# Optimization experiments

Measured on AMD Instinct MI355X. Metric: run time of the kernel, lower is better.

The kernel has to match this reference:

```python
import jax, jax.numpy as jnp
import numpy as np

KH, KW = 3, 3
K = KH * KW
PAD, STRIDE, DIL = 1, 1, 1


def _conv(x, w, b):
    y = jax.lax.conv_general_dilated(
        x, w, (STRIDE, STRIDE), ((PAD, PAD), (PAD, PAD)),
        rhs_dilation=(DIL, DIL), dimension_numbers=('NCHW', 'OIHW', 'NCHW'))
    return y + b[None, :, None, None]


def _bilinear_gather(x, py, px):
    # x: [B,C,H,W]; py, px: float sample coords [B,K,Ho,Wo]. Zero outside bounds.
    B, C, H, W = x.shape
    y0 = jnp.floor(py)
    x0 = jnp.floor(px)
    wy1 = py - y0
    wx1 = px - x0
    wy0 = 1.0 - wy1
    wx0 = 1.0 - wx1
    xf = x.reshape(B, C, H * W)

    def g(yi, xi):
        valid = (yi >= 0) & (yi < H) & (xi >= 0) & (xi < W)
        yc = jnp.clip(yi, 0, H - 1).astype(jnp.int32)
        xc = jnp.clip(xi, 0, W - 1).astype(jnp.int32)
        idx = (yc * W + xc).reshape(B, -1)                      # [B, K*Ho*Wo]
        v = jax.vmap(lambda im, ix: im[:, ix])(xf, idx)         # [B, C, K*Ho*Wo]
        v = v.reshape(B, C, *yi.shape[1:])                      # [B,C,K,Ho,Wo]
        return v * valid[:, None].astype(x.dtype)

    return ((wy0 * wx0)[:, None] * g(y0, x0)
            + (wy0 * wx1)[:, None] * g(y0, x0 + 1)
            + (wy1 * wx0)[:, None] * g(y0 + 1, x0)
            + (wy1 * wx1)[:, None] * g(y0 + 1, x0 + 1))


def setup_inputs() -> dict:
    key = jax.random.key(0)
    k1, k2, k3 = jax.random.split(key, 3)
    B, C, H, W = 8, 256, 64, 64
    x = jax.random.normal(k1, (B, C, H, W), dtype=jnp.float32)
    # small init for offset/mask conv so predicted offsets stay modest (as in DCNv2 practice)
    w_om = jax.random.normal(k2, (3 * K, C, KH, KW), dtype=jnp.float32) * 0.01
    b_om = jnp.zeros((3 * K,), dtype=jnp.float32)
    w_dc = jax.random.normal(k3, (C, C, KH, KW), dtype=jnp.float32) * (1.0 / np.sqrt(C * K))
    b_dc = jnp.zeros((C,), dtype=jnp.float32)
    return {"x": x, "w_om": w_om, "b_om": b_om, "w_dc": w_dc, "b_dc": b_dc}


def reference(x, w_om, b_om, w_dc, b_dc):
    B, C, H, W = x.shape
    om = _conv(x, w_om, b_om)                      # [B, 3K, H, W]
    offset = om[:, :2 * K].reshape(B, K, 2, H, W)  # per-tap (dy, dx)
    mask = jax.nn.sigmoid(om[:, 2 * K:])           # [B, K, H, W]
    dy, dx = offset[:, :, 0], offset[:, :, 1]
    kh = jnp.repeat(jnp.arange(KH), KW)            # [K] kernel row index
    kw = jnp.tile(jnp.arange(KW), KH)              # [K] kernel col index
    ho = jnp.arange(H)
    wo = jnp.arange(W)
    py = ho[None, None, :, None] * STRIDE - PAD + kh[None, :, None, None] * DIL + dy
    px = wo[None, None, None, :] * STRIDE - PAD + kw[None, :, None, None] * DIL + dx
    sampled = _bilinear_gather(x, py, px)          # [B,C,K,H,W]
    sampled = sampled * mask[:, None]              # modulated (DCNv2)
    w = w_dc.reshape(w_dc.shape[0], C, K)
    out = jnp.einsum('bckhw,ock->bohw', sampled, w) + b_dc[None, :, None, None]
    return out
```

## Files before the change

kernel.cpp:

```cpp
#include <hip/hip_runtime.h>
#include <hip/hip_bf16.h>
#include <hip/hip_fp16.h>
#include <math.h>

#define BB   8
#define CIN  256
#define HH   64
#define WW   64
#define OMC  27
#define HW   (HH*WW)
#define KTOT (CIN*9)
#define NPIX 32
#define SPITCH 296
#define SSZ   (NPIX*SPITCH)
#define XP1    40
#define TPW    17
#define TBUF   4096

typedef short bf16x8 __attribute__((ext_vector_type(8)));
typedef float f32x4  __attribute__((ext_vector_type(4)));

__device__ __forceinline__ unsigned short f2bf(float f) {
    union { float f; unsigned int u; } v; v.f = f;
    unsigned int r = v.u + 0x7FFFu + ((v.u >> 16) & 1u);
    return (unsigned short)(r >> 16);
}
__device__ __forceinline__ float bflo(unsigned int a) {
    union { unsigned int u; float f; } c; c.u = a << 16; return c.f;
}
__device__ __forceinline__ float bfhi(unsigned int a) {
    union { unsigned int u; float f; } c; c.u = a & 0xFFFF0000u; return c.f;
}

__global__ __launch_bounds__(256) void wprep_kernel(
    const float* __restrict__ w_dc, unsigned short* __restrict__ wA)
{
    int e = blockIdx.x * 256 + threadIdx.x;
    int o = e / KTOT;
    int k = e - o * KTOT;
    int c   = k / 9;
    int tap = k - c * 9;
    int kp  = (c >> 5) * 288 + tap * 32 + (c & 31);
    wA[((size_t)(kp >> 3) * 256 + o) * 8 + (kp & 7)] = f2bf(w_dc[e]);
}

__global__ __launch_bounds__(256) void womprep_kernel(
    const float* __restrict__ w_om, unsigned short* __restrict__ wOmA)
{
    int e = blockIdx.x * 256 + threadIdx.x;
    int j  = e & 7;
    int t1 = e >> 3;
    int o  = t1 & 31;
    int t2 = t1 >> 5;
    int cb = t2 & 3;
    int t3 = t2 >> 2;
    int cc = t3 & 7;
    int tap = t3 >> 3;
    int c = cc * 32 + cb * 8 + j;
    float v = (o < OMC) ? w_om[(size_t)o * KTOT + c * 9 + tap] : 0.f;
    wOmA[e] = f2bf(v);
}

__global__ __launch_bounds__(512, 4) void deform_mfma_kernel(
    const float* __restrict__ x, const unsigned short* __restrict__ wOmA,
    const float* __restrict__ b_om,
    const unsigned short* __restrict__ wA, const float* __restrict__ b_dc,
    float* __restrict__ out)
{
    const int rawb = blockIdx.x;
    const int obid = ((rawb & 7) << 7) | (rawb >> 3);
    const int b    = obid >> 7;
    const int h    = (obid >> 1) & 63;
    const int w0   = (obid & 1) * NPIX;
    const int t    = threadIdx.x;
    const int wv   = t >> 6;
    const int lane = t & 63;
    const int lq   = lane >> 4;
    const int lm   = lane & 15;

    __shared__ __align__(16) unsigned short sS[2 * SSZ];
    __shared__ __align__(16) unsigned short sR[2 * TBUF * 2];
    __shared__ __align__(16) int4 s_par[9 * NPIX];

    float* som  = reinterpret_cast<float*>(sS);
    unsigned short* bufA = sR;
    unsigned short* bufB = sR + 4080;

    const size_t xb_base = (size_t)b * CIN * HW;
    const float* gx_base = x + xb_base;

    int stg[7];
#pragma unroll
    for (int i = 0; i < 7; ++i) {
        int n = t + i * 512;
        if (n < 3200) {
            int slot = n / 200;
            int rc   = n - slot * 200;
            int r    = rc / 40;
            int c    = rc - r * 40;
            int gy   = min(max(h - 2 + r, 0), HH - 1);
            int gx   = min(max(w0 - 4 + c, 0), WW - 1);
            stg[i] = (rc * TPW + slot) | (slot << 12) | ((gy * WW + gx) << 16);
        } else stg[i] = -1;
    }

    {
        f32x4 accOm = (f32x4)(0.f);
        const int mfp = (wv >> 1) & 1;
        const int nfp = wv & 1;
        const int p   = nfp * 16 + lm;
        const bf16x8* wOmV = reinterpret_cast<const bf16x8*>(wOmA);

        auto stage1 = [&](int cc, unsigned short* dst) {
            const float* gch = gx_base + (size_t)cc * 32 * HW;
#pragma unroll
            for (int i = 0; i < 7; ++i) {
                int e = t + i * 512;
                if (e < 3264) {
                    int cl  = e / 102;
                    int rc  = e - cl * 102;
                    int row = rc / 34;
                    int col = rc - row * 34;
                    int gy  = h - 1 + row;
                    int gxx = w0 - 1 + col;
                    float v = 0.f;
                    if (gy >= 0 && gy < HH && (unsigned)gxx < WW)
                        v = gch[cl * HW + gy * WW + gxx];
                    dst[rc * XP1 + cl] = f2bf(v);
                }
            }
        };

        stage1(0, bufA);
        __syncthreads();
        for (int cc = 0; cc < 8; ++cc) {
            unsigned short* cur = (cc & 1) ? bufB : bufA;
            unsigned short* nxt = (cc & 1) ? bufA : bufB;
            if (cc < 7) stage1(cc + 1, nxt);
#pragma unroll
            for (int tap = 0; tap < 9; ++tap) {
                int kh = tap / 3, kw = tap % 3;
                bf16x8 bfr = *reinterpret_cast<const bf16x8*>(
                    &cur[(kh * 34 + p + kw) * XP1 + lq * 8]);
                bf16x8 af = wOmV[(((tap * 8 + cc) * 4 + lq) * 32) + mfp * 16 + lm];
                accOm = __builtin_amdgcn_mfma_f32_16x16x32_bf16(af, bfr, accOm, 0, 0, 0);
            }
            __syncthreads();
        }

        if (wv < 4) {
#pragma unroll
            for (int r = 0; r < 4; ++r) {
                int o = mfp * 16 + lq * 4 + r;
                if (o < OMC)
                    som[o * NPIX + p] = accOm[r] + b_om[o];
            }
        }
    }
    __syncthreads();

    unsigned int* tWw = reinterpret_cast<unsigned int*>(sR);
    const unsigned int* tW = tWw;

    float L0[7], L1[7];
    auto issueStage = [&](int ch) {
        const float* gch = gx_base + (size_t)ch * 32 * HW;
#pragma unroll
        for (int i = 0; i < 7; ++i)
            if (stg[i] >= 0) {
                int sl = (stg[i] >> 12) & 0xF;
                int go = (stg[i] >> 16) & 0xFFF;
                L0[i] = gch[(size_t)(2 * sl) * HW + go];
                L1[i] = gch[(size_t)(2 * sl + 1) * HW + go];
            }
    };
    auto writeTile = [&](int buf) {
        int off = buf << 12;
#pragma unroll
        for (int i = 0; i < 7; ++i)
            if (stg[i] >= 0)
                tWw[off + (stg[i] & 0xFFF)] =
                    f2bf(L0[i]) | ((unsigned int)f2bf(L1[i]) << 16);
    };

    const int pix  = t >> 4;
    const int slot = t & 15;

    auto gather = [&](int ch) {
        const int toff = (ch & 1) << 12;
        unsigned short* sSc = sS + (ch & 1) * SSZ;
#pragma unroll 3
        for (int tap = 0; tap < 9; ++tap) {
            int idx = tap * NPIX + pix;
            int4 pv = s_par[idx];
            int pk  = pv.x;
            float2 wab = __half22float2(*reinterpret_cast<__half2*>(&pv.y));
            float2 wcd = __half22float2(*reinterpret_cast<__half2*>(&pv.z));
            float v0, v1;
            if (pk >= 0) {
                int base = toff + (pk & 0xFF) * TPW + slot;
                unsigned int a00 = tW[base];
                unsigned int a01 = tW[base + TPW];
                unsigned int a10 = tW[base + 40 * TPW];
                unsigned int a11 = tW[base + 41 * TPW];
                v0 = wab.x * bflo(a00) + wab.y * bflo(a01)
                   + wcd.x * bflo(a10) + wcd.y * bflo(a11);
                v1 = wab.x * bfhi(a00) + wab.y * bfhi(a01)
                   + wcd.x * bfhi(a10) + wcd.y * bfhi(a11);
            } else {
                int off00 = (pk >> 10) & 0xFFF;
                int d01 = (pk >> 8) & 1;
                int d10 = ((pk >> 9) & 1) * WW;
                const float* xc = x + xb_base + (size_t)(ch * 32 + 2 * slot) * HW;
                v0 = wab.x * xc[off00]       + wab.y * xc[off00 + d01]
                   + wcd.x * xc[off00 + d10] + wcd.y * xc[off00 + d10 + d01];
                xc += HW;
                v1 = wab.x * xc[off00]       + wab.y * xc[off00 + d01]
                   + wcd.x * xc[off00 + d10] + wcd.y * xc[off00 + d10 + d01];
            }
            *reinterpret_cast<unsigned int*>(
                &sSc[pix * SPITCH + tap * 32 + 2 * slot]) =
                f2bf(v0) | ((unsigned int)f2bf(v1) << 16);
        }
    };

    issueStage(0);

    for (int i = t; i < 1392; i += 512) {
        int w = (i < 696) ? (3400 + i) : (4096 + 3400 + (i - 696));
        tWw[w] = 0u;
    }

    if (t < 9 * NPIX) {
        int tap = t >> 5;
        int pix2 = t & 31;
        float dy = som[(2 * tap) * NPIX + pix2];
        float dx = som[(2 * tap + 1) * NPIX + pix2];
        float mv = som[(18 + tap) * NPIX + pix2];
        float m  = 1.f / (1.f + expf(-mv));
        float py = (float)(h - 1 + tap / 3) + dy;
        float px = (float)(w0 + pix2 - 1 + tap % 3) + dx;
        float y0f = floorf(py), x0f = floorf(px);
        float wy1 = py - y0f, wx1 = px - x0f;
        float wy0 = 1.f - wy1, wx0 = 1.f - wx1;
        int y0 = (int)y0f, x0 = (int)x0f;
        int y1 = y0 + 1, x1 = x0 + 1;
        bool yv0 = (y0 >= 0) && (y0 < HH);
        bool yv1 = (y1 >= 0) && (y1 < HH);
        bool xv0 = (x0 >= 0) && (x0 < WW);
        bool xv1 = (x1 >= 0) && (x1 < WW);
        int yc0 = min(max(y0, 0), HH - 1), yc1 = min(max(y1, 0), HH - 1);
        int xc0 = min(max(x0, 0), WW - 1), xc1 = min(max(x1, 0), WW - 1);
        float wwx = (yv0 && xv0) ? wy0 * wx0 * m : 0.f;
        float wwy = (yv0 && xv1) ? wy0 * wx1 * m : 0.f;
        float wwz = (yv1 && xv0) ? wy1 * wx0 * m : 0.f;
        float www = (yv1 && xv1) ? wy1 * wx1 * m : 0.f;
        if (xc1 == xc0) { wwx += wwy; wwy = 0.f; wwz += www; www = 0.f; }
        if (yc1 == yc0) { wwx += wwz; wwz = 0.f; wwy += www; www = 0.f; }
        bool inT = (yc0 >= h - 2) && (yc1 <= h + 2) &&
                   (xc0 >= w0 - 4) && (xc1 <= w0 + 35);
        int lb = (yc0 - (h - 2)) * 40 + (xc0 - (w0 - 4));
        int pk = (lb & 0xFF) | ((xc1 - xc0) << 8) | ((yc1 - yc0) << 9)
               | ((yc0 * WW + xc0) << 10);
        if (!inT) pk |= (int)0x80000000;
        __half2 wab = __floats2half2_rn(wwx, wwy);
        __half2 wcd = __floats2half2_rn(wwz, www);
        s_par[t] = make_int4(pk,
                             *reinterpret_cast<int*>(&wab),
                             *reinterpret_cast<int*>(&wcd), 0);
    }
    writeTile(0);
    __syncthreads();

    gather(0);
    issueStage(1);
    writeTile(1);
    __syncthreads();

    f32x4 acc[2][2];
#pragma unroll
    for (int i = 0; i < 2; ++i)
#pragma unroll
        for (int j = 0; j < 2; ++j)
            acc[i][j] = (f32x4)(0.f);

    const bf16x8* wAv = reinterpret_cast<const bf16x8*>(wA);

    for (int ch = 0; ch < 8; ++ch) {
        if (ch < 6) issueStage(ch + 2);
        if (ch < 7) gather(ch + 1);

        const unsigned short* sSc = sS + (ch & 1) * SSZ;
        const int kb_base = ch * 36;
#pragma unroll 1
        for (int ks = 0; ks < 9; ++ks) {
            bf16x8 bfr[2];
#pragma unroll
            for (int nf = 0; nf < 2; ++nf)
                bfr[nf] = *reinterpret_cast<const bf16x8*>(
                    &sSc[(nf * 16 + lm) * SPITCH + ks * 32 + lq * 8]);
#pragma unroll
            for (int mf = 0; mf < 2; ++mf) {
                int o  = wv * 32 + mf * 16 + lm;
                int kb = kb_base + ks * 4 + lq;
                bf16x8 af = wAv[(size_t)kb * 256 + o];
#pragma unroll
                for (int nf = 0; nf < 2; ++nf)
                    acc[mf][nf] = __builtin_amdgcn_mfma_f32_16x16x32_bf16(
                        af, bfr[nf], acc[mf][nf], 0, 0, 0);
            }
        }

        if (ch < 6) writeTile(ch & 1);
        __syncthreads();
    }

#pragma unroll
    for (int mf = 0; mf < 2; ++mf) {
#pragma unroll
        for (int r = 0; r < 4; ++r) {
            int o = wv * 32 + mf * 16 + lq * 4 + r;
            float bo = b_dc[o];
#pragma unroll
            for (int nf = 0; nf < 2; ++nf) {
                int p = nf * 16 + lm;
                out[((size_t)(b * 256 + o)) * HW + h * WW + w0 + p] = acc[mf][nf][r] + bo;
            }
        }
    }
}

extern "C" void kernel_launch(void* const* d_in, const int* in_sizes, int n_in,
                              void* d_out, int out_size, void* d_ws, size_t ws_size,
                              hipStream_t stream) {
    const float* x    = (const float*)d_in[0];
    const float* w_om = (const float*)d_in[1];
    const float* b_om = (const float*)d_in[2];
    const float* w_dc = (const float*)d_in[3];
    const float* b_dc = (const float*)d_in[4];
    float* out = (float*)d_out;

    unsigned short* wA   = (unsigned short*)d_ws;
    unsigned short* wOmA = (unsigned short*)((char*)d_ws + 1179648);

    wprep_kernel<<<(256 * KTOT) / 256, 256, 0, stream>>>(w_dc, wA);
    womprep_kernel<<<73728 / 256, 256, 0, stream>>>(w_om, wOmA);
    deform_mfma_kernel<<<BB * HH * 2, 512, 0, stream>>>(x, wOmA, b_om, wA, b_dc, out);
}
```

Before: 156.0 us.

## Process full 64-pixel rows per block and single-buffer the sampled tile

```diff
diff --git a/kernel.cpp b/kernel.cpp
--- a/kernel.cpp
+++ b/kernel.cpp
@@ -10,12 +10,13 @@
 #define OMC  27
 #define HW   (HH*WW)
 #define KTOT (CIN*9)
-#define NPIX 32
+#define NPIX 64
 #define SPITCH 296
-#define SSZ   (NPIX*SPITCH)
 #define XP1    40
 #define TPW    17
-#define TBUF   4096
+#define TCOLS  72
+#define TRC    360
+#define TGUARD 7360
 
 typedef short bf16x8 __attribute__((ext_vector_type(8)));
 typedef float f32x4  __attribute__((ext_vector_type(4)));
@@ -68,61 +69,60 @@
     float* __restrict__ out)
 {
     const int rawb = blockIdx.x;
-    const int obid = ((rawb & 7) << 7) | (rawb >> 3);
-    const int b    = obid >> 7;
-    const int h    = (obid >> 1) & 63;
-    const int w0   = (obid & 1) * NPIX;
+    const int obid = ((rawb & 7) << 6) | (rawb >> 3);
+    const int b    = obid >> 6;
+    const int h    = obid & 63;
     const int t    = threadIdx.x;
     const int wv   = t >> 6;
     const int lane = t & 63;
     const int lq   = lane >> 4;
     const int lm   = lane & 15;
 
-    __shared__ __align__(16) unsigned short sS[2 * SSZ];
-    __shared__ __align__(16) unsigned short sR[2 * TBUF * 2];
+    __shared__ __align__(16) unsigned short sS[NPIX * SPITCH];
+    __shared__ __align__(16) unsigned short sR[15840];
     __shared__ __align__(16) int4 s_par[9 * NPIX];
 
     float* som  = reinterpret_cast<float*>(sS);
     unsigned short* bufA = sR;
-    unsigned short* bufB = sR + 4080;
+    unsigned short* bufB = sR + 7920;
 
     const size_t xb_base = (size_t)b * CIN * HW;
     const float* gx_base = x + xb_base;
 
-    int stg[7];
-#pragma unroll
-    for (int i = 0; i < 7; ++i) {
+    int stg[12];
+#pragma unroll
+    for (int i = 0; i < 12; ++i) {
         int n = t + i * 512;
-        if (n < 3200) {
-            int slot = n / 200;
-            int rc   = n - slot * 200;
-            int r    = rc / 40;
-            int c    = rc - r * 40;
+        if (n < TRC * 16) {
+            int slot = n & 15;
+            int rc   = n >> 4;
+            int r    = rc / TCOLS;
+            int c    = rc - r * TCOLS;
             int gy   = min(max(h - 2 + r, 0), HH - 1);
-            int gx   = min(max(w0 - 4 + c, 0), WW - 1);
-            stg[i] = (rc * TPW + slot) | (slot << 12) | ((gy * WW + gx) << 16);
+            int gx   = min(max(c - 4, 0), WW - 1);
+            stg[i] = (rc * TPW + slot) | (slot << 13) | ((gy * WW + gx) << 17);
         } else stg[i] = -1;
     }
 
     {
         f32x4 accOm = (f32x4)(0.f);
-        const int mfp = (wv >> 1) & 1;
-        const int nfp = wv & 1;
+        const int mfp = wv >> 2;
+        const int nfp = wv & 3;
         const int p   = nfp * 16 + lm;
         const bf16x8* wOmV = reinterpret_cast<const bf16x8*>(wOmA);
 
         auto stage1 = [&](int cc, unsigned short* dst) {
             const float* gch = gx_base + (size_t)cc * 32 * HW;
 #pragma unroll
-            for (int i = 0; i < 7; ++i) {
+            for (int i = 0; i < 13; ++i) {
                 int e = t + i * 512;
-                if (e < 3264) {
-                    int cl  = e / 102;
-                    int rc  = e - cl * 102;
-                    int row = rc / 34;
-                    int col = rc - row * 34;
+                if (e < 3 * 66 * 32) {
+                    int cl  = e / 198;
+                    int rc  = e - cl * 198;
+                    int row = rc / 66;
+                    int col = rc - row * 66;
                     int gy  = h - 1 + row;
-                    int gxx = w0 - 1 + col;
+                    int gxx = col - 1;
                     float v = 0.f;
                     if (gy >= 0 && gy < HH && (unsigned)gxx < WW)
                         v = gch[cl * HW + gy * WW + gxx];
@@ -141,20 +141,18 @@
             for (int tap = 0; tap < 9; ++tap) {
                 int kh = tap / 3, kw = tap % 3;
                 bf16x8 bfr = *reinterpret_cast<const bf16x8*>(
-                    &cur[(kh * 34 + p + kw) * XP1 + lq * 8]);
+                    &cur[(kh * 66 + p + kw) * XP1 + lq * 8]);
                 bf16x8 af = wOmV[(((tap * 8 + cc) * 4 + lq) * 32) + mfp * 16 + lm];
                 accOm = __builtin_amdgcn_mfma_f32_16x16x32_bf16(af, bfr, accOm, 0, 0, 0);
             }
             __syncthreads();
         }
 
-        if (wv < 4) {
-#pragma unroll
-            for (int r = 0; r < 4; ++r) {
-                int o = mfp * 16 + lq * 4 + r;
-                if (o < OMC)
-                    som[o * NPIX + p] = accOm[r] + b_om[o];
-            }
+#pragma unroll
+        for (int r = 0; r < 4; ++r) {
+            int o = mfp * 16 + lq * 4 + r;
+            if (o < OMC)
+                som[o * NPIX + p] = accOm[r] + b_om[o];
         }
     }
     __syncthreads();
@@ -162,84 +160,39 @@
     unsigned int* tWw = reinterpret_cast<unsigned int*>(sR);
     const unsigned int* tW = tWw;
 
-    float L0[7], L1[7];
+    float L0[12], L1[12];
     auto issueStage = [&](int ch) {
         const float* gch = gx_base + (size_t)ch * 32 * HW;
 #pragma unroll
-        for (int i = 0; i < 7; ++i)
+        for (int i = 0; i < 12; ++i)
             if (stg[i] >= 0) {
-                int sl = (stg[i] >> 12) & 0xF;
-                int go = (stg[i] >> 16) & 0xFFF;
+                int sl = (stg[i] >> 13) & 0xF;
+                int go = (stg[i] >> 17) & 0xFFF;
                 L0[i] = gch[(size_t)(2 * sl) * HW + go];
                 L1[i] = gch[(size_t)(2 * sl + 1) * HW + go];
             }
     };
-    auto writeTile = [&](int buf) {
-        int off = buf << 12;
-#pragma unroll
-        for (int i = 0; i < 7; ++i)
+    auto writeTile = [&]() {
+#pragma unroll
+        for (int i = 0; i < 12; ++i)
             if (stg[i] >= 0)
-                tWw[off + (stg[i] & 0xFFF)] =
+                tWw[stg[i] & 0x1FFF] =
                     f2bf(L0[i]) | ((unsigned int)f2bf(L1[i]) << 16);
     };
 
-    const int pix  = t >> 4;
-    const int slot = t & 15;
-
-    auto gather = [&](int ch) {
-        const int toff = (ch & 1) << 12;
-        unsigned short* sSc = sS + (ch & 1) * SSZ;
-#pragma unroll 3
-        for (int tap = 0; tap < 9; ++tap) {
-            int idx = tap * NPIX + pix;
-            int4 pv = s_par[idx];
-            int pk  = pv.x;
-            float2 wab = __half22float2(*reinterpret_cast<__half2*>(&pv.y));
-            float2 wcd = __half22float2(*reinterpret_cast<__half2*>(&pv.z));
-            float v0, v1;
-            if (pk >= 0) {
-                int base = toff + (pk & 0xFF) * TPW + slot;
-                unsigned int a00 = tW[base];
-                unsigned int a01 = tW[base + TPW];
-                unsigned int a10 = tW[base + 40 * TPW];
-                unsigned int a11 = tW[base + 41 * TPW];
-                v0 = wab.x * bflo(a00) + wab.y * bflo(a01)
-                   + wcd.x * bflo(a10) + wcd.y * bflo(a11);
-                v1 = wab.x * bfhi(a00) + wab.y * bfhi(a01)
-                   + wcd.x * bfhi(a10) + wcd.y * bfhi(a11);
-            } else {
-                int off00 = (pk >> 10) & 0xFFF;
-                int d01 = (pk >> 8) & 1;
-                int d10 = ((pk >> 9) & 1) * WW;
-                const float* xc = x + xb_base + (size_t)(ch * 32 + 2 * slot) * HW;
-                v0 = wab.x * xc[off00]       + wab.y * xc[off00 + d01]
-                   + wcd.x * xc[off00 + d10] + wcd.y * xc[off00 + d10 + d01];
-                xc += HW;
-                v1 = wab.x * xc[off00]       + wab.y * xc[off00 + d01]
-                   + wcd.x * xc[off00 + d10] + wcd.y * xc[off00 + d10 + d01];
-            }
-            *reinterpret_cast<unsigned int*>(
-                &sSc[pix * SPITCH + tap * 32 + 2 * slot]) =
-                f2bf(v0) | ((unsigned int)f2bf(v1) << 16);
-        }
-    };
-
     issueStage(0);
 
-    for (int i = t; i < 1392; i += 512) {
-        int w = (i < 696) ? (3400 + i) : (4096 + 3400 + (i - 696));
-        tWw[w] = 0u;
-    }
-
-    if (t < 9 * NPIX) {
-        int tap = t >> 5;
-        int pix2 = t & 31;
-        float dy = som[(2 * tap) * NPIX + pix2];
-        float dx = som[(2 * tap + 1) * NPIX + pix2];
-        float mv = som[(18 + tap) * NPIX + pix2];
+    for (int i = t; i < 1240; i += 512) tWw[6120 + i] = 0u;
+
+    for (int e = t; e < 9 * NPIX; e += 512) {
+        int tap = e / NPIX;
+        int pix = e - tap * NPIX;
+        float dy = som[(2 * tap) * NPIX + pix];
+        float dx = som[(2 * tap + 1) * NPIX + pix];
+        float mv = som[(18 + tap) * NPIX + pix];
         float m  = 1.f / (1.f + expf(-mv));
         float py = (float)(h - 1 + tap / 3) + dy;
-        float px = (float)(w0 + pix2 - 1 + tap % 3) + dx;
+        float px = (float)(pix - 1 + tap % 3) + dx;
         float y0f = floorf(py), x0f = floorf(px);
         float wy1 = py - y0f, wx1 = px - x0f;
         float wy0 = 1.f - wy1, wx0 = 1.f - wx1;
@@ -257,61 +210,93 @@
         float www = (yv1 && xv1) ? wy1 * wx1 * m : 0.f;
         if (xc1 == xc0) { wwx += wwy; wwy = 0.f; wwz += www; www = 0.f; }
         if (yc1 == yc0) { wwx += wwz; wwz = 0.f; wwy += www; www = 0.f; }
-        bool inT = (yc0 >= h - 2) && (yc1 <= h + 2) &&
-                   (xc0 >= w0 - 4) && (xc1 <= w0 + 35);
-        int lb = (yc0 - (h - 2)) * 40 + (xc0 - (w0 - 4));
-        int pk = (lb & 0xFF) | ((xc1 - xc0) << 8) | ((yc1 - yc0) << 9)
-               | ((yc0 * WW + xc0) << 10);
+        bool inT = (yc0 >= h - 2) && (yc1 <= h + 2);
+        int lb = (yc0 - (h - 2)) * TCOLS + (xc0 + 4);
+        int pk = (lb & 0x3FF) | ((xc1 - xc0) << 10) | ((yc1 - yc0) << 11)
+               | ((yc0 * WW + xc0) << 12);
         if (!inT) pk |= (int)0x80000000;
         __half2 wab = __floats2half2_rn(wwx, wwy);
         __half2 wcd = __floats2half2_rn(wwz, www);
-        s_par[t] = make_int4(pk,
+        s_par[e] = make_int4(pk,
                              *reinterpret_cast<int*>(&wab),
                              *reinterpret_cast<int*>(&wcd), 0);
     }
-    writeTile(0);
+    writeTile();
     __syncthreads();
 
-    gather(0);
-    issueStage(1);
-    writeTile(1);
-    __syncthreads();
-
-    f32x4 acc[2][2];
+    f32x4 acc[2][4];
 #pragma unroll
     for (int i = 0; i < 2; ++i)
 #pragma unroll
-        for (int j = 0; j < 2; ++j)
+        for (int j = 0; j < 4; ++j)
             acc[i][j] = (f32x4)(0.f);
 
+    const int slot    = t & 15;
+    const int pixpair = t >> 4;
     const bf16x8* wAv = reinterpret_cast<const bf16x8*>(wA);
 
     for (int ch = 0; ch < 8; ++ch) {
-        if (ch < 6) issueStage(ch + 2);
-        if (ch < 7) gather(ch + 1);
-
-        const unsigned short* sSc = sS + (ch & 1) * SSZ;
+#pragma unroll 1
+        for (int px2 = 0; px2 < 2; ++px2) {
+            int pix = pixpair + 32 * px2;
+#pragma unroll 3
+            for (int tap = 0; tap < 9; ++tap) {
+                int4 pv = s_par[tap * NPIX + pix];
+                int pk  = pv.x;
+                float2 wab = __half22float2(*reinterpret_cast<__half2*>(&pv.y));
+                float2 wcd = __half22float2(*reinterpret_cast<__half2*>(&pv.z));
+                float v0, v1;
+                if (pk >= 0) {
+                    int base = (pk & 0x3FF) * TPW + slot;
+                    unsigned int a00 = tW[base];
+                    unsigned int a01 = tW[base + TPW];
+                    unsigned int a10 = tW[base + TCOLS * TPW];
+                    unsigned int a11 = tW[base + (TCOLS + 1) * TPW];
+                    v0 = wab.x * bflo(a00) + wab.y * bflo(a01)
+                       + wcd.x * bflo(a10) + wcd.y * bflo(a11);
+                    v1 = wab.x * bfhi(a00) + wab.y * bfhi(a01)
+                       + wcd.x * bfhi(a10) + wcd.y * bfhi(a11);
+                } else {
+                    int off00 = (pk >> 12) & 0xFFF;
+                    int d01 = (pk >> 10) & 1;
+                    int d10 = ((pk >> 11) & 1) * WW;
+                    const float* xc = x + xb_base + (size_t)(ch * 32 + 2 * slot) * HW;
+                    v0 = wab.x * xc[off00]       + wab.y * xc[off00 + d01]
+                       + wcd.x * xc[off00 + d10] + wcd.y * xc[off00 + d10 + d01];
+                    xc += HW;
+                    v1 = wab.x * xc[off00]       + wab.y * xc[off00 + d01]
+                       + wcd.x * xc[off00 + d10] + wcd.y * xc[off00 + d10 + d01];
+                }
+                *reinterpret_cast<unsigned int*>(
+                    &sS[pix * SPITCH + tap * 32 + 2 * slot]) =
+                    f2bf(v0) | ((unsigned int)f2bf(v1) << 16);
+            }
+        }
+        __syncthreads();
+
+        if (ch < 7) issueStage(ch + 1);
+
         const int kb_base = ch * 36;
 #pragma unroll 1
         for (int ks = 0; ks < 9; ++ks) {
-            bf16x8 bfr[2];
-#pragma unroll
-            for (int nf = 0; nf < 2; ++nf)
+            bf16x8 bfr[4];
+#pragma unroll
+            for (int nf = 0; nf < 4; ++nf)
                 bfr[nf] = *reinterpret_cast<const bf16x8*>(
-                    &sSc[(nf * 16 + lm) * SPITCH + ks * 32 + lq * 8]);
+                    &sS[(nf * 16 + lm) * SPITCH + ks * 32 + lq * 8]);
 #pragma unroll
             for (int mf = 0; mf < 2; ++mf) {
                 int o  = wv * 32 + mf * 16 + lm;
                 int kb = kb_base + ks * 4 + lq;
                 bf16x8 af = wAv[(size_t)kb * 256 + o];
 #pragma unroll
-                for (int nf = 0; nf < 2; ++nf)
+                for (int nf = 0; nf < 4; ++nf)
                     acc[mf][nf] = __builtin_amdgcn_mfma_f32_16x16x32_bf16(
                         af, bfr[nf], acc[mf][nf], 0, 0, 0);
             }
         }
 
-        if (ch < 6) writeTile(ch & 1);
+        if (ch < 7) writeTile();
         __syncthreads();
     }
 
@@ -322,9 +307,9 @@
             int o = wv * 32 + mf * 16 + lq * 4 + r;
             float bo = b_dc[o];
 #pragma unroll
-            for (int nf = 0; nf < 2; ++nf) {
+            for (int nf = 0; nf < 4; ++nf) {
                 int p = nf * 16 + lm;
-                out[((size_t)(b * 256 + o)) * HW + h * WW + w0 + p] = acc[mf][nf][r] + bo;
+                out[((size_t)(b * 256 + o)) * HW + h * WW + p] = acc[mf][nf][r] + bo;
             }
         }
     }
@@ -345,5 +330,5 @@
 
     wprep_kernel<<<(256 * KTOT) / 256, 256, 0, stream>>>(w_dc, wA);
     womprep_kernel<<<73728 / 256, 256, 0, stream>>>(w_om, wOmA);
-    deform_mfma_kernel<<<BB * HH * 2, 512, 0, stream>>>(x, wOmA, b_om, wA, b_dc, out);
-}
+    deform_mfma_kernel<<<BB * HH, 512, 0, stream>>>(x, wOmA, b_om, wA, b_dc, out);
+}
```

Measured after the change: 191.6 us. 1.23x slower.
